# Kernel optimization log

Measured on AMD Instinct MI355X. Metric: run time of the kernel, lower is better.

The kernel has to match this reference:

```python
import jax, jax.numpy as jnp
import numpy as np
import math

C = 96; HEADS = 3; HD = C // HEADS; WS = 8; B = 4; H = 256; W = 256
EPS = 1e-5; SCALE = HD ** -0.5; LOGIT_MAX = math.log(1.0 / 0.01)
N = WS * WS


def _rel_pos():
    coords = np.stack(np.meshgrid(np.arange(WS), np.arange(WS), indexing='ij')).reshape(2, -1)
    rel = (coords[:, :, None] - coords[:, None, :]).transpose(1, 2, 0).astype(np.float32)
    return jnp.asarray(np.sign(rel) * np.log1p(np.abs(rel)))  # [N, N, 2]

REL = _rel_pos()


def conv1x1(x, w, b):
    return jnp.einsum('bchw,oc->bohw', x, w) + b[None, :, None, None]


def dwconv(x, w, b, pad, reflect=False):
    if reflect:
        x = jnp.pad(x, ((0, 0), (0, 0), (pad, pad), (pad, pad)), mode='reflect')
        padding = 'VALID'
    else:
        padding = [(pad, pad), (pad, pad)]
    y = jax.lax.conv_general_dilated(x, w, (1, 1), padding,
                                     feature_group_count=x.shape[1],
                                     dimension_numbers=('NCHW', 'OIHW', 'NCHW'))
    return y + b[None, :, None, None]


def window_partition(x):  # [B,H,W,C] -> [nW, WS*WS, C]
    b, h, w, c = x.shape
    x = x.reshape(b, h // WS, WS, w // WS, WS, c).transpose(0, 1, 3, 2, 4, 5)
    return x.reshape(-1, WS * WS, c)


def window_reverse(win, h, w):  # [nW, WS*WS, C] -> [B,H,W,C]
    b = win.shape[0] // ((h // WS) * (w // WS))
    x = win.reshape(b, h // WS, w // WS, WS, WS, -1).transpose(0, 1, 3, 2, 4, 5)
    return x.reshape(b, h, w, -1)


def setup_inputs() -> dict:
    key = jax.random.key(0)
    ks = jax.random.split(key, 16)
    def nrm(k, shape, std=0.02):
        return jax.random.normal(k, shape, jnp.float32) * std
    inp = {'x': jax.random.normal(ks[0], (B, C, H, W), jnp.float32)}
    inp.update(
        agn_weight=jnp.ones((C,), jnp.float32), agn_bias=jnp.zeros((C,), jnp.float32),
        meta1_w=nrm(ks[1], (C,)), meta1_b=jnp.ones((C,), jnp.float32),
        meta2_w=nrm(ks[2], (C,)), meta2_b=jnp.zeros((C,), jnp.float32),
        la1_w=nrm(ks[3], (C, 1, 3, 3)), la1_b=jnp.zeros((C,), jnp.float32),
        la2_w=nrm(ks[4], (C, 1, 3, 3)), la2_b=jnp.zeros((C,), jnp.float32),
        ta1_w=nrm(ks[5], (C, 1, 3, 3)), ta1_b=jnp.zeros((C,), jnp.float32),
        ta2_w=nrm(ks[6], (C, 1, 3, 3)), ta2_b=jnp.zeros((C,), jnp.float32),
        q_w=nrm(ks[7], (C, C)), q_b=jnp.zeros((C,), jnp.float32),
        kv_w=nrm(ks[8], (2 * C, C)), kv_b=jnp.zeros((2 * C,), jnp.float32),
        dw_w=nrm(ks[9], (C, 1, 5, 5)), dw_b=jnp.zeros((C,), jnp.float32),
        proj_w=nrm(ks[10], (C, C)), proj_b=jnp.zeros((C,), jnp.float32),
        logit_scale=jnp.asarray(math.log(1.0 / 0.07), jnp.float32),
        rp_w1=nrm(ks[11], (256, 2)), rp_b1=jnp.zeros((256,), jnp.float32),
        rp_w2=nrm(ks[12], (HEADS, 256)), rp_b2=jnp.zeros((HEADS,), jnp.float32),
        m1_w=nrm(ks[13], (4 * C, C)), m1_b=jnp.zeros((4 * C,), jnp.float32),
        m2_w=nrm(ks[14], (C, 4 * C)), m2_b=jnp.zeros((C,), jnp.float32),
    )
    return inp


def reference(x, agn_weight, agn_bias, meta1_w, meta1_b, meta2_w, meta2_b,
              la1_w, la1_b, la2_w, la2_b, ta1_w, ta1_b, ta2_w, ta2_b,
              q_w, q_b, kv_w, kv_b, dw_w, dw_b, proj_w, proj_b,
              logit_scale, rp_w1, rp_b1, rp_w2, rp_b2,
              m1_w, m1_b, m2_w, m2_b):
    identity = x
    # ---- AGN: per-sample global mean/std norm + dynamic affine + two dw-conv branches
    mean = jnp.mean(x, axis=(1, 2, 3), keepdims=True)                      # [B,1,1,1]
    std = jnp.sqrt(jnp.mean((x - mean) ** 2, axis=(1, 2, 3), keepdims=True) + EPS)
    xn = (x - mean) / std
    rescale = std * meta1_w[None, :, None, None] + meta1_b[None, :, None, None]   # conv1x1(1->C) on std
    rebias = mean * meta2_w[None, :, None, None] + meta2_b[None, :, None, None]
    local = dwconv(jax.nn.relu(dwconv(xn, la1_w, la1_b, 1)), la2_w, la2_b, 1)
    texture = dwconv(jax.nn.relu(dwconv(xn, ta1_w, ta1_b, 1)), ta2_w, ta2_b, 1)
    xn = xn * (agn_weight[None, :, None, None] * rescale) + (agn_bias[None, :, None, None] + rebias) + local + texture
    # ---- DSAttention (use_attn, DWConv, shift_size=0, H%WS==0 so no padding)
    Q = conv1x1(xn, q_w, q_b)
    KV = conv1x1(xn, kv_w, kv_b)                                           # [B,2C,H,W]
    qkv_img = jnp.concatenate([Q, KV], axis=1).transpose(0, 2, 3, 1)       # [B,H,W,3C]
    co = dwconv(Q, dw_w, dw_b, 2, reflect=True).transpose(0, 2, 3, 1)      # reflect-padded 5x5 dwconv
    qkv = window_partition(qkv_img)                                        # [nW,N,3C]
    cw = window_partition(co)                                              # [nW,N,C]
    nW = qkv.shape[0]
    qkv = qkv.reshape(nW, N, 3, HEADS, HD).transpose(2, 0, 3, 1, 4)        # [3,nW,h,N,hd]
    q = cw.reshape(nW, N, HEADS, HD).transpose(0, 2, 1, 3)                 # q replaced by conv branch
    k = qkv[1] * SCALE
    v = qkv[2]
    ls = jnp.exp(jnp.minimum(logit_scale, LOGIT_MAX))
    hb = jax.nn.relu(REL @ rp_w1.T + rp_b1)                                # [N,N,256]
    bias = (hb @ rp_w2.T + rp_b2).transpose(2, 0, 1)                       # [h,N,N]
    attn = jax.nn.softmax(jnp.einsum('whnd,whmd->whnm', q, k) * ls + bias[None], axis=-1)
    o = jnp.einsum('whnm,whmd->whnd', attn, v).transpose(0, 2, 1, 3).reshape(nW, N, C)
    out = window_reverse(o, x.shape[2], x.shape[3]).transpose(0, 3, 1, 2)  # [B,C,H,W]
    a = conv1x1(out, proj_w, proj_b)
    x = identity + a * rescale + rebias
    # ---- MLP (1x1 conv -> ReLU -> 1x1 conv), residual
    x = x + conv1x1(jax.nn.relu(conv1x1(x, m1_w, m1_b)), m2_w, m2_b)
    return x
```

## Files before the change

### kernel.cpp

```cpp
#include <hip/hip_runtime.h>
#include <hip/hip_bf16.h>

typedef __hip_bfloat16 bf16;

#define PER_B     6291456
#define EPS_F     1e-5f
#define SCALE_F   0.17677669529663687f
#define LOGIT_MAX_F 4.605170185988092f

__device__ __forceinline__ float b2f(bf16 v){ return __bfloat162float(v); }
__device__ __forceinline__ bf16  f2b(float v){ return __float2bfloat16(v); }

template<int DT> __device__ __forceinline__ float rdf(const void* p, size_t i){
  return DT ? ((const float*)p)[i] : b2f(((const bf16*)p)[i]);
}
template<int DT> __device__ __forceinline__ void wrf(void* p, size_t i, float v){
  if (DT) ((float*)p)[i] = v; else ((bf16*)p)[i] = f2b(v);
}
template<int DT> __device__ __forceinline__ float2 rd2(const void* p, size_t i){
  if (DT) return *(const float2*)((const float*)p + i);
  unsigned u = *(const unsigned*)((const bf16*)p + i);
  return make_float2(__uint_as_float(u << 16), __uint_as_float(u & 0xffff0000u));
}

typedef __attribute__((ext_vector_type(8))) short short8v;
typedef __attribute__((ext_vector_type(4))) short short4v;
typedef __attribute__((ext_vector_type(4))) float f32x4;

__device__ __forceinline__ short f2bs(float v){
  unsigned u = __float_as_uint(v);
  return (short)((u + 0x7fffu + ((u >> 16) & 1u)) >> 16);
}
__device__ __forceinline__ float bs2f(short s){
  return __uint_as_float(((unsigned)(unsigned short)s) << 16);
}

template<int DT> __device__ __forceinline__ short8v ld8(const void* p, size_t i){
  short8v a;
  if (DT){
    const float* f = (const float*)p + i;
    float4 lo = *(const float4*)f;
    float4 hi = *(const float4*)(f + 4);
    a[0]=f2bs(lo.x); a[1]=f2bs(lo.y); a[2]=f2bs(lo.z); a[3]=f2bs(lo.w);
    a[4]=f2bs(hi.x); a[5]=f2bs(hi.y); a[6]=f2bs(hi.z); a[7]=f2bs(hi.w);
  } else {
    a = *(const short8v*)((const short*)p + i);
  }
  return a;
}
template<int DT> __device__ __forceinline__ short8v ld4x2(const void* p, size_t i0){
  short8v a;
  if (DT){
    const float* f = (const float*)p;
    float4 lo = *(const float4*)(f + i0);
    float4 hi = *(const float4*)(f + i0 + 16);
    a[0]=f2bs(lo.x); a[1]=f2bs(lo.y); a[2]=f2bs(lo.z); a[3]=f2bs(lo.w);
    a[4]=f2bs(hi.x); a[5]=f2bs(hi.y); a[6]=f2bs(hi.z); a[7]=f2bs(hi.w);
  } else {
    const short* s = (const short*)p;
    short4v lo = *(const short4v*)(s + i0);
    short4v hi = *(const short4v*)(s + i0 + 16);
    a[0]=lo[0]; a[1]=lo[1]; a[2]=lo[2]; a[3]=lo[3];
    a[4]=hi[0]; a[5]=hi[1]; a[6]=hi[2]; a[7]=hi[3];
  }
  return a;
}

__global__ __launch_bounds__(256) void k_detect(const void* __restrict__ x, int* __restrict__ flag){
  __shared__ int cnt;
  if (threadIdx.x == 0) cnt = 0;
  __syncthreads();
  float v = b2f(((const bf16*)x)[(size_t)threadIdx.x * 16]);
  int bad = (!(v == v)) || (fabsf(v) > 1e20f);
  if (bad) atomicAdd(&cnt, 1);
  __syncthreads();
  if (threadIdx.x == 0) *flag = (cnt >= 4) ? 1 : 0;
}

template<int DT>
__global__ __launch_bounds__(256) void k_stats_partial(const void* __restrict__ x,
    float* __restrict__ partials, const int* __restrict__ flag){
  if (*flag != DT) return;
  int blk = blockIdx.x;
  int b = blk >> 8, chunk = blk & 255;
  const int chunkN = PER_B / 256;
  size_t base = (size_t)b * PER_B + (size_t)chunk * chunkN;
  float s = 0.f, ss = 0.f;
  if (DT){
    const float4* p4 = (const float4*)((const float*)x + base);
    for (int i = threadIdx.x; i < chunkN/4; i += 256){
      float4 v = p4[i];
      s  += v.x + v.y + v.z + v.w;
      ss += v.x*v.x + v.y*v.y + v.z*v.z + v.w*v.w;
    }
  } else {
    const short8v* p8 = (const short8v*)((const short*)x + base);
    for (int i = threadIdx.x; i < chunkN/8; i += 256){
      short8v v = p8[i];
      #pragma unroll
      for (int k = 0; k < 8; k++){
        float f = bs2f(v[k]); s += f; ss += f*f;
      }
    }
  }
  __shared__ float sh[512];
  sh[threadIdx.x] = s; sh[256 + threadIdx.x] = ss;
  __syncthreads();
  for (int st = 128; st > 0; st >>= 1){
    if (threadIdx.x < st){
      sh[threadIdx.x]     += sh[threadIdx.x + st];
      sh[256+threadIdx.x] += sh[256+threadIdx.x + st];
    }
    __syncthreads();
  }
  if (threadIdx.x == 0){ partials[blk*2] = sh[0]; partials[blk*2+1] = sh[256]; }
}

template<int DT>
__global__ __launch_bounds__(256) void k_stats_final(const float* __restrict__ partials,
    const void* m1w, const void* m1b, const void* m2w, const void* m2b,
    float* __restrict__ stats, const int* __restrict__ flag){
  if (*flag != DT) return;
  __shared__ float sh[512];
  __shared__ float mS[4], sS[4];
  for (int b = 0; b < 4; b++){
    sh[threadIdx.x]     = partials[(b*256+threadIdx.x)*2];
    sh[256+threadIdx.x] = partials[(b*256+threadIdx.x)*2+1];
    __syncthreads();
    for (int st = 128; st > 0; st >>= 1){
      if (threadIdx.x < st){
        sh[threadIdx.x]     += sh[threadIdx.x + st];
        sh[256+threadIdx.x] += sh[256+threadIdx.x + st];
      }
      __syncthreads();
    }
    if (threadIdx.x == 0){
      float mean = sh[0] / (float)PER_B;
      float var  = sh[256] / (float)PER_B - mean*mean;
      float stdv = sqrtf(var + EPS_F);
      mS[b] = mean; sS[b] = stdv;
      stats[b] = mean; stats[4+b] = stdv;
    }
    __syncthreads();
  }
  for (int t = threadIdx.x; t < 384; t += 256){
    int b = t / 96, c = t % 96;
    stats[8+t]   = sS[b]*rdf<DT>(m1w,c) + rdf<DT>(m1b,c);
    stats[392+t] = mS[b]*rdf<DT>(m2w,c) + rdf<DT>(m2b,c);
  }
}

template<int DT>
__global__ __launch_bounds__(256) void k_bias(const void* w1, const void* b1v,
    const void* w2, const void* b2v, float* __restrict__ biasT, const int* __restrict__ flag){
  if (*flag != DT) return;
  int i = blockIdx.x >> 6, j = blockIdx.x & 63;
  int dy = (i>>3) - (j>>3), dx = (i&7) - (j&7);
  float fy = (float)dy, fx = (float)dx;
  float r0 = copysignf(log1pf(fabsf(fy)), fy);
  float r1 = copysignf(log1pf(fabsf(fx)), fx);
  int t = threadIdx.x;
  int wv = t >> 6, ln = t & 63;
  float hb = fmaxf(r0*rdf<DT>(w1,t*2) + r1*rdf<DT>(w1,t*2+1) + rdf<DT>(b1v,t), 0.f);
  __shared__ float ps[3][4];
  #pragma unroll
  for (int h = 0; h < 3; h++){
    float v = hb * rdf<DT>(w2, h*256+t);
    v += __shfl_down(v, 32);
    v += __shfl_down(v, 16);
    v += __shfl_down(v, 8);
    v += __shfl_down(v, 4);
    v += __shfl_down(v, 2);
    v += __shfl_down(v, 1);
    if (ln == 0) ps[h][wv] = v;
  }
  __syncthreads();
  if (t < 3)
    biasT[t*4096 + j*64 + i] = ps[t][0]+ps[t][1]+ps[t][2]+ps[t][3] + rdf<DT>(b2v, t);
}

template<int DT>
__global__ __launch_bounds__(256) void k_agn_fused(const void* __restrict__ x,
    const float* __restrict__ stats,
    const void* la1w, const void* la1b, const void* la2w, const void* la2b,
    const void* ta1w, const void* ta1b, const void* ta2w, const void* ta2b,
    const void* agnw, const void* agnb,
    bf16* __restrict__ xn2, const int* __restrict__ flag){
  if (*flag != DT) return;
  __shared__ float xs[1296];
  __shared__ float ts[1156];
  __shared__ float us[1156];
  int idx = blockIdx.x;
  int tile = idx & 63; int bc = idx >> 6; int c = bc % 96; int b = bc / 96;
  int oy = (tile >> 3) << 5, ox = (tile & 7) << 5;
  float mean = stats[b], sd = stats[4+b];
  size_t xbase = ((size_t)bc) << 16;
  for (int it = threadIdx.x; it < 1296; it += 256){
    int ly = it / 36, lx = it % 36;
    int gy = oy - 2 + ly, gx = ox - 2 + lx;
    float v = 0.f;
    if (gy >= 0 && gy < 256 && gx >= 0 && gx < 256)
      v = (rdf<DT>(x, xbase + (gy<<8) + gx) - mean) / sd;
    xs[it] = v;
  }
  float wl1[9], wt1[9], wl2[9], wt2[9];
  #pragma unroll
  for (int k = 0; k < 9; k++){
    wl1[k] = rdf<DT>(la1w, c*9+k); wt1[k] = rdf<DT>(ta1w, c*9+k);
    wl2[k] = rdf<DT>(la2w, c*9+k); wt2[k] = rdf<DT>(ta2w, c*9+k);
  }
  float bl1 = rdf<DT>(la1b, c), bt1 = rdf<DT>(ta1b, c);
  __syncthreads();
  for (int it = threadIdx.x; it < 1156; it += 256){
    int ly = it / 34, lx = it % 34;
    int cy = oy - 1 + ly, cx = ox - 1 + lx;
    float a1 = 0.f, a2 = 0.f;
    if (cy >= 0 && cy < 256 && cx >= 0 && cx < 256){
      a1 = bl1; a2 = bt1;
      #pragma unroll
      for (int dy = 0; dy < 3; dy++)
        #pragma unroll
        for (int dx = 0; dx < 3; dx++){
          float v = xs[(ly+dy)*36 + lx+dx];
          a1 += v * wl1[dy*3+dx]; a2 += v * wt1[dy*3+dx];
        }
      a1 = fmaxf(a1, 0.f); a2 = fmaxf(a2, 0.f);
    }
    ts[it] = a1; us[it] = a2;
  }
  __syncthreads();
  float agw = rdf<DT>(agnw,c)*stats[8+bc];
  float agb = rdf<DT>(agnb,c) + stats[392+bc];
  float bl2 = rdf<DT>(la2b, c), bt2 = rdf<DT>(ta2b, c);
  #pragma unroll
  for (int k = 0; k < 4; k++){
    int px = threadIdx.x + (k << 8);
    int ly = px >> 5, lx = px & 31;
    float l = bl2, t = bt2;
    #pragma unroll
    for (int dy = 0; dy < 3; dy++)
      #pragma unroll
      for (int dx = 0; dx < 3; dx++){
        l += ts[(ly+dy)*34 + lx+dx] * wl2[dy*3+dx];
        t += us[(ly+dy)*34 + lx+dx] * wt2[dy*3+dx];
      }
    float v = xs[(ly+2)*36 + lx+2];
    float r = v*agw + agb + l + t;
    xn2[xbase + ((oy+ly)<<8) + ox + lx] = f2b(r);
  }
}

#define CS_OFF 0
#define XS_OFF 13312
#define QB_OFF 43264
#define KT_OFF 13312
#define VD_OFF 26624
#define XC_OFF 40448
#define PS_OFF 40448
#define OS_OFF 13312

template<int DT>
__global__ __launch_bounds__(256, 3) void k_attn_mega(const bf16* __restrict__ xn2,
    const void* qw, const void* qb, const void* kvw, const void* kvb,
    const void* dww, const void* dwb, const void* pw, const void* pb,
    const void* lsin, const float* __restrict__ biasT,
    const void* __restrict__ xin, const float* __restrict__ stats,
    void* __restrict__ outp, const int* __restrict__ flag){
  if (*flag != DT) return;
  __shared__ __align__(16) char smem[53760];
  int tid = threadIdx.x, wid = blockIdx.x;
  int b = wid >> 10, wy = (wid >> 5) & 31, wx = wid & 31;
  int wv = tid >> 6, ln = tid & 63;
  int r = ln & 15, q = ln >> 4;

  {
    short* xs = (short*)(smem + XS_OFF);
    if (wy >= 1 && wy <= 30 && wx >= 1 && wx <= 30){
      for (int it = tid; it < 13824; it += 256){
        int t = it % 144, craw = it / 144;
        int c = craw ^ ((t >> 3) & 7);
        int ty = (wy<<3) - 2 + t/12, tx = (wx<<3) - 2 + t%12;
        xs[t*104 + c] = ((const short*)xn2)[(((size_t)(b*96 + c))<<16) + (ty<<8) + tx];
      }
    } else {
      for (int it = tid; it < 13824; it += 256){
        int t = it % 144, craw = it / 144;
        int c = craw ^ ((t >> 3) & 7);
        int ty = (wy<<3) - 2 + t/12, tx = (wx<<3) - 2 + t%12;
        ty = ty < 0 ? -ty : (ty > 255 ? 510 - ty : ty);
        tx = tx < 0 ? -tx : (tx > 255 ? 510 - tx : tx);
        xs[t*104 + c] = ((const short*)xn2)[(((size_t)(b*96 + c))<<16) + (ty<<8) + tx];
      }
    }
  }
  __syncthreads();

  {
    const short* xs = (const short*)(smem + XS_OFF);
    short* Qb = (short*)(smem + QB_OFF) + wv*1184;
    short* cs = (short*)(smem + CS_OFF);
    int ty0 = (ln>>3)+2, tx0 = (ln&7)+2;
    for (int mt = wv; mt < 6; mt += 4){
      short8v aw[3];
      #pragma unroll
      for (int kt = 0; kt < 3; kt++)
        aw[kt] = ld8<DT>(qw, (size_t)(16*mt + r)*96 + 32*kt + 8*q);
      float qb4[4];
      #pragma unroll
      for (int j = 0; j < 4; j++) qb4[j] = rdf<DT>(qb, 16*mt + 4*q + j);
      float accs[9][4];
      #pragma unroll
      for (int nt = 0; nt < 9; nt++){
        f32x4 acc = {0.f,0.f,0.f,0.f};
        #pragma unroll
        for (int kt = 0; kt < 3; kt++){
          short8v bx = *(const short8v*)(xs + (16*nt + r)*104 + 32*kt + 8*q);
          acc = __builtin_amdgcn_mfma_f32_16x16x32_bf16(aw[kt], bx, acc, 0, 0, 0);
        }
        #pragma unroll
        for (int j = 0; j < 4; j++) accs[nt][j] = acc[j] + qb4[j];
      }
      if (q < 2){
        #pragma unroll
        for (int nt = 0; nt < 9; nt++)
          #pragma unroll
          for (int j = 0; j < 4; j++)
            Qb[(4*q+j)*148 + 16*nt + r] = f2bs(accs[nt][j]);
      }
      asm volatile("s_waitcnt lgkmcnt(0)" ::: "memory");
      for (int cl = 0; cl < 8; cl++){
        int c = 16*mt + cl;
        float a = rdf<DT>(dwb, c);
        #pragma unroll
        for (int dy = -2; dy <= 2; dy++)
          #pragma unroll
          for (int dx = -2; dx <= 2; dx++)
            a += bs2f(Qb[cl*148 + (ty0+dy)*12 + tx0+dx]) * rdf<DT>(dww, c*25 + (dy+2)*5 + dx+2);
        cs[ln*104 + c] = f2bs(a);
      }
      asm volatile("s_waitcnt lgkmcnt(0)" ::: "memory");
      if (q >= 2){
        #pragma unroll
        for (int nt = 0; nt < 9; nt++)
          #pragma unroll
          for (int j = 0; j < 4; j++)
            Qb[(4*(q-2)+j)*148 + 16*nt + r] = f2bs(accs[nt][j]);
      }
      asm volatile("s_waitcnt lgkmcnt(0)" ::: "memory");
      for (int cl = 8; cl < 16; cl++){
        int c = 16*mt + cl;
        float a = rdf<DT>(dwb, c);
        #pragma unroll
        for (int dy = -2; dy <= 2; dy++)
          #pragma unroll
          for (int dx = -2; dx <= 2; dx++)
            a += bs2f(Qb[(cl-8)*148 + (ty0+dy)*12 + tx0+dx]) * rdf<DT>(dww, c*25 + (dy+2)*5 + dx+2);
        cs[ln*104 + c] = f2bs(a);
      }
      asm volatile("s_waitcnt lgkmcnt(0)" ::: "memory");
    }
  }
  __syncthreads();

  {
    short* xc = (short*)(smem + XC_OFF);
    for (int it = tid; it < 768; it += 256){
      int c = it >> 3, row = it & 7;
      const short* src = (const short*)xn2 + (((size_t)(b*96 + c))<<16)
                         + (((wy<<3)+row)<<8) + (wx<<3);
      short8v v = *(const short8v*)src;
      #pragma unroll
      for (int k = 0; k < 8; k++){
        int pe = k ^ row;
        xc[(row*8+pe)*104 + c] = v[pe];
      }
    }
  }
  __syncthreads();
  {
    const short* xc = (const short*)(smem + XC_OFF);
    short* Kt = (short*)(smem + KT_OFF);
    short* Vd = (short*)(smem + VD_OFF);
    for (int mtk = wv; mtk < 12; mtk += 4){
      short8v aw[3];
      #pragma unroll
      for (int kt = 0; kt < 3; kt++)
        aw[kt] = ld8<DT>(kvw, (size_t)(16*mtk + r)*96 + 32*kt + 8*q);
      float bb[4];
      #pragma unroll
      for (int j = 0; j < 4; j++) bb[j] = rdf<DT>(kvb, 16*mtk + 4*q + j);
      for (int nt = 0; nt < 4; nt++){
        f32x4 acc = {0.f,0.f,0.f,0.f};
        #pragma unroll
        for (int kt = 0; kt < 3; kt++){
          short8v bx = *(const short8v*)(xc + (16*nt + r)*104 + 32*kt + 8*q);
          acc = __builtin_amdgcn_mfma_f32_16x16x32_bf16(aw[kt], bx, acc, 0, 0, 0);
        }
        if (mtk < 6){
          short4v kv;
          #pragma unroll
          for (int j = 0; j < 4; j++) kv[j] = f2bs((acc[j] + bb[j]) * SCALE_F);
          *(short4v*)(Kt + (16*nt + r)*104 + 16*mtk + 4*q) = kv;
        } else {
          #pragma unroll
          for (int j = 0; j < 4; j++)
            Vd[(16*(mtk-6) + 4*q + j)*72 + 16*nt + r] = f2bs(acc[j] + bb[j]);
        }
      }
    }
  }
  __syncthreads();

  float o_save[24];
  {
    const short* cs = (const short*)(smem + CS_OFF);
    const short* Kt = (const short*)(smem + KT_OFF);
    const short* Vd = (const short*)(smem + VD_OFF);
    short* Psw = (short*)(smem + PS_OFF) + wv*1152;
    float lsv = __expf(fminf(rdf<DT>(lsin, 0), LOGIT_MAX_F));
    #pragma unroll
    for (int h = 0; h < 3; h++){
      short8v qa = *(const short8v*)(cs + (16*wv + r)*104 + 32*h + 8*q);
      f32x4 s[4];
      #pragma unroll
      for (int mt = 0; mt < 4; mt++){
        short8v kb = *(const short8v*)(Kt + (16*mt + r)*104 + 32*h + 8*q);
        f32x4 z = {0.f,0.f,0.f,0.f};
        s[mt] = __builtin_amdgcn_mfma_f32_16x16x32_bf16(qa, kb, z, 0, 0, 0);
      }
      float l[4][4];
      #pragma unroll
      for (int mt = 0; mt < 4; mt++){
        float4 bv = *(const float4*)(biasT + h*4096 + (16*mt + r)*64 + 16*wv + 4*q);
        l[mt][0] = s[mt][0]*lsv + bv.x;
        l[mt][1] = s[mt][1]*lsv + bv.y;
        l[mt][2] = s[mt][2]*lsv + bv.z;
        l[mt][3] = s[mt][3]*lsv + bv.w;
      }
      float mx[4], sm[4];
      #pragma unroll
      for (int j = 0; j < 4; j++){
        float m0 = fmaxf(fmaxf(l[0][j], l[1][j]), fmaxf(l[2][j], l[3][j]));
        m0 = fmaxf(m0, __shfl_xor(m0, 1));
        m0 = fmaxf(m0, __shfl_xor(m0, 2));
        m0 = fmaxf(m0, __shfl_xor(m0, 4));
        m0 = fmaxf(m0, __shfl_xor(m0, 8));
        mx[j] = m0; sm[j] = 0.f;
      }
      #pragma unroll
      for (int mt = 0; mt < 4; mt++)
        #pragma unroll
        for (int j = 0; j < 4; j++){
          float p = __expf(l[mt][j] - mx[j]);
          sm[j] += p;
          Psw[(4*q+j)*72 + 16*mt + r] = f2bs(p);
        }
      #pragma unroll
      for (int j = 0; j < 4; j++){
        sm[j] += __shfl_xor(sm[j], 1);
        sm[j] += __shfl_xor(sm[j], 2);
        sm[j] += __shfl_xor(sm[j], 4);
        sm[j] += __shfl_xor(sm[j], 8);
      }
      float inv[4];
      #pragma unroll
      for (int j = 0; j < 4; j++) inv[j] = 1.f / sm[j];
      asm volatile("s_waitcnt lgkmcnt(0)" ::: "memory");
      short8v pa0 = *(const short8v*)(Psw + r*72 + 8*q);
      short8v pa1 = *(const short8v*)(Psw + r*72 + 32 + 8*q);
      #pragma unroll
      for (int dt = 0; dt < 2; dt++){
        f32x4 o = {0.f,0.f,0.f,0.f};
        short8v vb0 = *(const short8v*)(Vd + (32*h + 16*dt + r)*72 + 8*q);
        short8v vb1 = *(const short8v*)(Vd + (32*h + 16*dt + r)*72 + 32 + 8*q);
        o = __builtin_amdgcn_mfma_f32_16x16x32_bf16(pa0, vb0, o, 0, 0, 0);
        o = __builtin_amdgcn_mfma_f32_16x16x32_bf16(pa1, vb1, o, 0, 0, 0);
        #pragma unroll
        for (int j = 0; j < 4; j++) o_save[h*8 + dt*4 + j] = o[j] * inv[j];
      }
      asm volatile("s_waitcnt lgkmcnt(0)" ::: "memory");
    }
  }
  __syncthreads();

  {
    short* os = (short*)(smem + OS_OFF);
    #pragma unroll
    for (int h = 0; h < 3; h++)
      #pragma unroll
      for (int dt = 0; dt < 2; dt++)
        #pragma unroll
        for (int j = 0; j < 4; j++)
          os[(16*wv + 4*q + j)*104 + 32*h + 16*dt + r] = f2bs(o_save[h*8 + dt*4 + j]);
  }
  __syncthreads();

  {
    const short* os = (const short*)(smem + OS_OFF);
    short8v ob[3];
    #pragma unroll
    for (int kt = 0; kt < 3; kt++)
      ob[kt] = *(const short8v*)(os + (16*wv + r)*104 + 32*kt + 8*q);
    for (int mt = 0; mt < 6; mt++){
      f32x4 acc = {0.f,0.f,0.f,0.f};
      #pragma unroll
      for (int kt = 0; kt < 3; kt++){
        short8v aw = ld8<DT>(pw, (size_t)(16*mt + r)*96 + 32*kt + 8*q);
        acc = __builtin_amdgcn_mfma_f32_16x16x32_bf16(aw, ob[kt], acc, 0, 0, 0);
      }
      #pragma unroll
      for (int j = 0; j < 4; j++){
        int oc = 16*mt + 4*q + j;
        int n  = 16*wv + r;
        int gy = (wy<<3) + (n>>3), gx = (wx<<3) + (n&7);
        size_t gi = (((size_t)(b*96 + oc))<<16) + (gy<<8) + gx;
        float a = acc[j] + rdf<DT>(pb, oc);
        float x1 = rdf<DT>(xin, gi) + a*stats[8 + b*96 + oc] + stats[392 + b*96 + oc];
        wrf<DT>(outp, gi, x1);
      }
    }
  }
}

template<int DT>
__global__ __launch_bounds__(256) void k_mlp_mfma(void* __restrict__ io,
    const void* w1, const void* b1, const void* w2, const void* b2v,
    const int* __restrict__ flag){
  if (*flag != DT) return;
  __shared__ __align__(16) short x1s[256*104];
  int blk = blockIdx.x; int b = blk >> 8; int pix0 = (blk & 255) << 8;
  int tid = threadIdx.x;

  for (int c = 0; c < 96; c++){
    size_t gi = (((size_t)(b*96 + c))<<16) + pix0 + tid;
    short v = DT ? f2bs(((const float*)io)[gi]) : ((const short*)io)[gi];
    x1s[tid*104 + c] = v;
  }
  __syncthreads();

  int wv = tid >> 6, l = tid & 63;
  int r = l & 15, q = l >> 4;
  int pbase = wv << 6;

  short8v bxs[3][4];
  #pragma unroll
  for (int kt = 0; kt < 3; kt++)
    #pragma unroll
    for (int nt = 0; nt < 4; nt++)
      bxs[kt][nt] = *(const short8v*)&x1s[(pbase + 16*nt + r)*104 + 32*kt + 8*q];

  f32x4 acc2[6][4];
  #pragma unroll
  for (int mt = 0; mt < 6; mt++)
    #pragma unroll
    for (int nt = 0; nt < 4; nt++)
      acc2[mt][nt] = (f32x4){0.f,0.f,0.f,0.f};

  #pragma unroll 2
  for (int t = 0; t < 12; t++){
    short8v aA[3], aB[3];
    #pragma unroll
    for (int kt = 0; kt < 3; kt++){
      aA[kt] = ld8<DT>(w1, (size_t)(32*t + r)*96      + 32*kt + 8*q);
      aB[kt] = ld8<DT>(w1, (size_t)(32*t + 16 + r)*96 + 32*kt + 8*q);
    }
    float bA[4], bB[4];
    #pragma unroll
    for (int j = 0; j < 4; j++){
      bA[j] = rdf<DT>(b1, 32*t + 4*q + j);
      bB[j] = rdf<DT>(b1, 32*t + 16 + 4*q + j);
    }
    f32x4 a1A[4], a1B[4];
    #pragma unroll
    for (int nt = 0; nt < 4; nt++){
      a1A[nt] = (f32x4){0.f,0.f,0.f,0.f};
      a1B[nt] = (f32x4){0.f,0.f,0.f,0.f};
    }
    #pragma unroll
    for (int kt = 0; kt < 3; kt++){
      #pragma unroll
      for (int nt = 0; nt < 4; nt++){
        a1A[nt] = __builtin_amdgcn_mfma_f32_16x16x32_bf16(aA[kt], bxs[kt][nt], a1A[nt], 0, 0, 0);
        a1B[nt] = __builtin_amdgcn_mfma_f32_16x16x32_bf16(aB[kt], bxs[kt][nt], a1B[nt], 0, 0, 0);
      }
    }
    short8v B2[4];
    #pragma unroll
    for (int nt = 0; nt < 4; nt++){
      short8v h;
      #pragma unroll
      for (int j = 0; j < 4; j++){
        h[j]   = f2bs(fmaxf(a1A[nt][j] + bA[j], 0.f));
        h[4+j] = f2bs(fmaxf(a1B[nt][j] + bB[j], 0.f));
      }
      B2[nt] = h;
    }
    #pragma unroll
    for (int mt = 0; mt < 6; mt++){
      short8v wA = ld4x2<DT>(w2, (size_t)(16*mt + r)*384 + 32*t + 4*q);
      #pragma unroll
      for (int nt = 0; nt < 4; nt++)
        acc2[mt][nt] = __builtin_amdgcn_mfma_f32_16x16x32_bf16(wA, B2[nt], acc2[mt][nt], 0, 0, 0);
    }
  }

  #pragma unroll
  for (int mt = 0; mt < 6; mt++)
    #pragma unroll
    for (int nt = 0; nt < 4; nt++)
      #pragma unroll
      for (int j = 0; j < 4; j++){
        int oc = 16*mt + 4*q + j;
        int pl = pbase + 16*nt + r;
        size_t gi = (((size_t)(b*96 + oc))<<16) + pix0 + pl;
        float v = acc2[mt][nt][j] + rdf<DT>(b2v, oc);
        if (DT){
          ((float*)io)[gi] = ((const float*)io)[gi] + v;
        } else {
          ((bf16*)io)[gi] = f2b(bs2f(x1s[pl*104 + oc]) + v);
        }
      }
}

extern "C" void kernel_launch(void* const* d_in, const int* in_sizes, int n_in,
                              void* d_out, int out_size, void* d_ws, size_t ws_size,
                              hipStream_t stream) {
  const void* x      = d_in[0];
  const void* agnw   = d_in[1];
  const void* agnb   = d_in[2];
  const void* meta1w = d_in[3];
  const void* meta1b = d_in[4];
  const void* meta2w = d_in[5];
  const void* meta2b = d_in[6];
  const void* la1w   = d_in[7];
  const void* la1b   = d_in[8];
  const void* la2w   = d_in[9];
  const void* la2b   = d_in[10];
  const void* ta1w   = d_in[11];
  const void* ta1b   = d_in[12];
  const void* ta2w   = d_in[13];
  const void* ta2b   = d_in[14];
  const void* qw     = d_in[15];
  const void* qb     = d_in[16];
  const void* kvw    = d_in[17];
  const void* kvb    = d_in[18];
  const void* dww    = d_in[19];
  const void* dwb    = d_in[20];
  const void* pw     = d_in[21];
  const void* pb     = d_in[22];
  const void* lsin   = d_in[23];
  const void* rpw1   = d_in[24];
  const void* rpb1   = d_in[25];
  const void* rpw2   = d_in[26];
  const void* rpb2   = d_in[27];
  const void* m1w    = d_in[28];
  const void* m1b    = d_in[29];
  const void* m2w    = d_in[30];
  const void* m2b    = d_in[31];

  char* ws = (char*)d_ws;
  int*   flag     = (int*)ws;
  float* partials = (float*)(ws + 256);
  float* stats    = (float*)(ws + 8448);
  float* biasT    = (float*)(ws + 12288);
  bf16*  xn2      = (bf16*)(ws + 65536);

  k_detect<<<1, 256, 0, stream>>>(x, flag);

  k_stats_partial<0><<<1024, 256, 0, stream>>>(x, partials, flag);
  k_stats_final<0>  <<<1,    256, 0, stream>>>(partials, meta1w, meta1b, meta2w, meta2b, stats, flag);
  k_bias<0>         <<<4096, 256, 0, stream>>>(rpw1, rpb1, rpw2, rpb2, biasT, flag);
  k_agn_fused<0>    <<<24576,256, 0, stream>>>(x, stats, la1w, la1b, la2w, la2b,
                                               ta1w, ta1b, ta2w, ta2b, agnw, agnb, xn2, flag);
  k_attn_mega<0>    <<<4096, 256, 0, stream>>>(xn2, qw, qb, kvw, kvb, dww, dwb, pw, pb,
                                               lsin, biasT, x, stats, d_out, flag);
  k_mlp_mfma<0>     <<<1024, 256, 0, stream>>>(d_out, m1w, m1b, m2w, m2b, flag);

  k_stats_partial<1><<<1024, 256, 0, stream>>>(x, partials, flag);
  k_stats_final<1>  <<<1,    256, 0, stream>>>(partials, meta1w, meta1b, meta2w, meta2b, stats, flag);
  k_bias<1>         <<<4096, 256, 0, stream>>>(rpw1, rpb1, rpw2, rpb2, biasT, flag);
  k_agn_fused<1>    <<<24576,256, 0, stream>>>(x, stats, la1w, la1b, la2w, la2b,
                                               ta1w, ta1b, ta2w, ta2b, agnw, agnb, xn2, flag);
  k_attn_mega<1>    <<<4096, 256, 0, stream>>>(xn2, qw, qb, kvw, kvb, dww, dwb, pw, pb,
                                               lsin, biasT, x, stats, d_out, flag);
  k_mlp_mfma<1>     <<<1024, 256, 0, stream>>>(d_out, m1w, m1b, m2w, m2b, flag);
}
```

Baseline: 1.011 ms.

## Store normalized intermediate channels-last so attention loads pixels with vector reads

The AGN kernel now processes 16x16 tiles with each wave looping over 24 channels and writes xn2 in NHWC order instead of NCHW. The attention kernel can then load each halo pixel's 96 channels with 16-byte vector loads rather than scalar gathers. It also builds the center-window tile from the already-staged halo in shared memory instead of rereading global memory. The trade-off is that the AGN writes become strided scalar bf16 stores across channels, and the grid shrinks to 1024 blocks with per-wave serial channel loops.

Measured after the change: 1.225 ms. 1.21x slower.

```diff
diff --git a/kernel.cpp b/kernel.cpp
--- a/kernel.cpp
+++ b/kernel.cpp
@@ -187,66 +187,69 @@
     const void* agnw, const void* agnb,
     bf16* __restrict__ xn2, const int* __restrict__ flag){
   if (*flag != DT) return;
-  __shared__ float xs[1296];
-  __shared__ float ts[1156];
-  __shared__ float us[1156];
+  __shared__ float smemf[4192];
   int idx = blockIdx.x;
-  int tile = idx & 63; int bc = idx >> 6; int c = bc % 96; int b = bc / 96;
-  int oy = (tile >> 3) << 5, ox = (tile & 7) << 5;
+  int tile = idx & 255; int b = idx >> 8;
+  int oy = (tile >> 4) << 4, ox = (tile & 15) << 4;
+  int wv = threadIdx.x >> 6, ln = threadIdx.x & 63;
+  float* xs = smemf + wv*1048;
+  float* ts = xs + 400;
+  float* us = ts + 324;
   float mean = stats[b], sd = stats[4+b];
-  size_t xbase = ((size_t)bc) << 16;
-  for (int it = threadIdx.x; it < 1296; it += 256){
-    int ly = it / 36, lx = it % 36;
-    int gy = oy - 2 + ly, gx = ox - 2 + lx;
-    float v = 0.f;
-    if (gy >= 0 && gy < 256 && gx >= 0 && gx < 256)
-      v = (rdf<DT>(x, xbase + (gy<<8) + gx) - mean) / sd;
-    xs[it] = v;
-  }
-  float wl1[9], wt1[9], wl2[9], wt2[9];
-  #pragma unroll
-  for (int k = 0; k < 9; k++){
-    wl1[k] = rdf<DT>(la1w, c*9+k); wt1[k] = rdf<DT>(ta1w, c*9+k);
-    wl2[k] = rdf<DT>(la2w, c*9+k); wt2[k] = rdf<DT>(ta2w, c*9+k);
-  }
-  float bl1 = rdf<DT>(la1b, c), bt1 = rdf<DT>(ta1b, c);
-  __syncthreads();
-  for (int it = threadIdx.x; it < 1156; it += 256){
-    int ly = it / 34, lx = it % 34;
-    int cy = oy - 1 + ly, cx = ox - 1 + lx;
-    float a1 = 0.f, a2 = 0.f;
-    if (cy >= 0 && cy < 256 && cx >= 0 && cx < 256){
-      a1 = bl1; a2 = bt1;
+  for (int c = wv*24; c < wv*24 + 24; c++){
+    size_t xbase = ((size_t)(b*96 + c)) << 16;
+    for (int it = ln; it < 400; it += 64){
+      int ly = it / 20, lx = it % 20;
+      int gy = oy - 2 + ly, gx = ox - 2 + lx;
+      float v = 0.f;
+      if (gy >= 0 && gy < 256 && gx >= 0 && gx < 256)
+        v = (rdf<DT>(x, xbase + (gy<<8) + gx) - mean) / sd;
+      xs[it] = v;
+    }
+    float wl1[9], wt1[9], wl2[9], wt2[9];
+    #pragma unroll
+    for (int k = 0; k < 9; k++){
+      wl1[k] = rdf<DT>(la1w, c*9+k); wt1[k] = rdf<DT>(ta1w, c*9+k);
+      wl2[k] = rdf<DT>(la2w, c*9+k); wt2[k] = rdf<DT>(ta2w, c*9+k);
+    }
+    float bl1 = rdf<DT>(la1b, c), bt1 = rdf<DT>(ta1b, c);
+    asm volatile("s_waitcnt lgkmcnt(0)" ::: "memory");
+    for (int it = ln; it < 324; it += 64){
+      int ly = it / 18, lx = it % 18;
+      int cy = oy - 1 + ly, cx = ox - 1 + lx;
+      float a1 = 0.f, a2 = 0.f;
+      if (cy >= 0 && cy < 256 && cx >= 0 && cx < 256){
+        a1 = bl1; a2 = bt1;
+        #pragma unroll
+        for (int dy = 0; dy < 3; dy++)
+          #pragma unroll
+          for (int dx = 0; dx < 3; dx++){
+            float v = xs[(ly+dy)*20 + lx+dx];
+            a1 += v * wl1[dy*3+dx]; a2 += v * wt1[dy*3+dx];
+          }
+        a1 = fmaxf(a1, 0.f); a2 = fmaxf(a2, 0.f);
+      }
+      ts[it] = a1; us[it] = a2;
+    }
+    float agw = rdf<DT>(agnw,c)*stats[8 + b*96 + c];
+    float agb = rdf<DT>(agnb,c) + stats[392 + b*96 + c];
+    float bl2 = rdf<DT>(la2b, c), bt2 = rdf<DT>(ta2b, c);
+    asm volatile("s_waitcnt lgkmcnt(0)" ::: "memory");
+    for (int it = ln; it < 256; it += 64){
+      int ly = it >> 4, lx = it & 15;
+      float l = bl2, t = bt2;
       #pragma unroll
       for (int dy = 0; dy < 3; dy++)
         #pragma unroll
         for (int dx = 0; dx < 3; dx++){
-          float v = xs[(ly+dy)*36 + lx+dx];
-          a1 += v * wl1[dy*3+dx]; a2 += v * wt1[dy*3+dx];
+          l += ts[(ly+dy)*18 + lx+dx] * wl2[dy*3+dx];
+          t += us[(ly+dy)*18 + lx+dx] * wt2[dy*3+dx];
         }
-      a1 = fmaxf(a1, 0.f); a2 = fmaxf(a2, 0.f);
-    }
-    ts[it] = a1; us[it] = a2;
-  }
-  __syncthreads();
-  float agw = rdf<DT>(agnw,c)*stats[8+bc];
-  float agb = rdf<DT>(agnb,c) + stats[392+bc];
-  float bl2 = rdf<DT>(la2b, c), bt2 = rdf<DT>(ta2b, c);
-  #pragma unroll
-  for (int k = 0; k < 4; k++){
-    int px = threadIdx.x + (k << 8);
-    int ly = px >> 5, lx = px & 31;
-    float l = bl2, t = bt2;
-    #pragma unroll
-    for (int dy = 0; dy < 3; dy++)
-      #pragma unroll
-      for (int dx = 0; dx < 3; dx++){
-        l += ts[(ly+dy)*34 + lx+dx] * wl2[dy*3+dx];
-        t += us[(ly+dy)*34 + lx+dx] * wt2[dy*3+dx];
-      }
-    float v = xs[(ly+2)*36 + lx+2];
-    float r = v*agw + agb + l + t;
-    xn2[xbase + ((oy+ly)<<8) + ox + lx] = f2b(r);
+      float v = xs[(ly+2)*20 + lx+2];
+      float r = v*agw + agb + l + t;
+      xn2[(((size_t)b<<16) + ((oy+ly)<<8) + ox + lx)*96 + c] = f2b(r);
+    }
+    asm volatile("s_waitcnt lgkmcnt(0)" ::: "memory");
   }
 }
 
@@ -275,21 +278,22 @@
 
   {
     short* xs = (short*)(smem + XS_OFF);
+    const short* xb = (const short*)xn2;
     if (wy >= 1 && wy <= 30 && wx >= 1 && wx <= 30){
-      for (int it = tid; it < 13824; it += 256){
-        int t = it % 144, craw = it / 144;
-        int c = craw ^ ((t >> 3) & 7);
-        int ty = (wy<<3) - 2 + t/12, tx = (wx<<3) - 2 + t%12;
-        xs[t*104 + c] = ((const short*)xn2)[(((size_t)(b*96 + c))<<16) + (ty<<8) + tx];
+      for (int it = tid; it < 1728; it += 256){
+        int px = it / 12, g = it - px*12;
+        int ty = (wy<<3) - 2 + px/12, tx = (wx<<3) - 2 + px%12;
+        short8v v = *(const short8v*)(xb + ((((size_t)b<<16) + (ty<<8) + tx)*96 + 8*g));
+        *(short8v*)(xs + px*104 + 8*g) = v;
       }
     } else {
-      for (int it = tid; it < 13824; it += 256){
-        int t = it % 144, craw = it / 144;
-        int c = craw ^ ((t >> 3) & 7);
-        int ty = (wy<<3) - 2 + t/12, tx = (wx<<3) - 2 + t%12;
+      for (int it = tid; it < 1728; it += 256){
+        int px = it / 12, g = it - px*12;
+        int ty = (wy<<3) - 2 + px/12, tx = (wx<<3) - 2 + px%12;
         ty = ty < 0 ? -ty : (ty > 255 ? 510 - ty : ty);
         tx = tx < 0 ? -tx : (tx > 255 ? 510 - tx : tx);
-        xs[t*104 + c] = ((const short*)xn2)[(((size_t)(b*96 + c))<<16) + (ty<<8) + tx];
+        short8v v = *(const short8v*)(xb + ((((size_t)b<<16) + (ty<<8) + tx)*96 + 8*g));
+        *(short8v*)(xs + px*104 + 8*g) = v;
       }
     }
   }
@@ -363,17 +367,22 @@
   __syncthreads();
 
   {
+    const short* xs = (const short*)(smem + XS_OFF);
     short* xc = (short*)(smem + XC_OFF);
-    for (int it = tid; it < 768; it += 256){
-      int c = it >> 3, row = it & 7;
-      const short* src = (const short*)xn2 + (((size_t)(b*96 + c))<<16)
-                         + (((wy<<3)+row)<<8) + (wx<<3);
-      short8v v = *(const short8v*)src;
-      #pragma unroll
-      for (int k = 0; k < 8; k++){
-        int pe = k ^ row;
-        xc[(row*8+pe)*104 + c] = v[pe];
-      }
+    short8v tmp[3];
+    #pragma unroll
+    for (int k = 0; k < 3; k++){
+      int it = tid + k*256;
+      int n = it / 12, g = it - n*12;
+      int t = ((n>>3)+2)*12 + (n&7) + 2;
+      tmp[k] = *(const short8v*)(xs + t*104 + 8*g);
+    }
+    __syncthreads();
+    #pragma unroll
+    for (int k = 0; k < 3; k++){
+      int it = tid + k*256;
+      int n = it / 12, g = it - n*12;
+      *(short8v*)(xc + n*104 + 8*g) = tmp[k];
     }
   }
   __syncthreads();
@@ -670,7 +679,7 @@
   k_stats_partial<0><<<1024, 256, 0, stream>>>(x, partials, flag);
   k_stats_final<0>  <<<1,    256, 0, stream>>>(partials, meta1w, meta1b, meta2w, meta2b, stats, flag);
   k_bias<0>         <<<4096, 256, 0, stream>>>(rpw1, rpb1, rpw2, rpb2, biasT, flag);
-  k_agn_fused<0>    <<<24576,256, 0, stream>>>(x, stats, la1w, la1b, la2w, la2b,
+  k_agn_fused<0>    <<<1024, 256, 0, stream>>>(x, stats, la1w, la1b, la2w, la2b,
                                                ta1w, ta1b, ta2w, ta2b, agnw, agnb, xn2, flag);
   k_attn_mega<0>    <<<4096, 256, 0, stream>>>(xn2, qw, qb, kvw, kvb, dww, dwb, pw, pb,
                                                lsin, biasT, x, stats, d_out, flag);
@@ -679,7 +688,7 @@
   k_stats_partial<1><<<1024, 256, 0, stream>>>(x, partials, flag);
   k_stats_final<1>  <<<1,    256, 0, stream>>>(partials, meta1w, meta1b, meta2w, meta2b, stats, flag);
   k_bias<1>         <<<4096, 256, 0, stream>>>(rpw1, rpb1, rpw2, rpb2, biasT, flag);
-  k_agn_fused<1>    <<<24576,256, 0, stream>>>(x, stats, la1w, la1b, la2w, la2b,
+  k_agn_fused<1>    <<<1024, 256, 0, stream>>>(x, stats, la1w, la1b, la2w, la2b,
                                                ta1w, ta1b, ta2w, ta2b, agnw, agnb, xn2, flag);
   k_attn_mega<1>    <<<4096, 256, 0, stream>>>(xn2, qw, qb, kvw, kvb, dww, dwb, pw, pb,
                                                lsin, biasT, x, stats, d_out, flag);
```
